# Kernel optimization log

Measured on AMD Instinct MI355X. Metric: run time of the kernel, lower is better.

Reference implementation:

```python
import jax, jax.numpy as jnp
import numpy as np

B, T, D, I, C, H = 8192, 128, 7, 128, 10, 64
L = 2 ** D
SUBSET = int(I * 0.8)  # feature_subset_size = 102


def setup_inputs() -> dict:
    key = jax.random.key(0)
    ks = jax.random.split(key, 7)
    x = jax.random.normal(ks[0], (B, I), dtype=jnp.float32)
    # exact feature-subset mask: SUBSET ones per (tree, depth) row
    r = jax.random.uniform(ks[1], (T, D, I))
    ranks = jnp.argsort(jnp.argsort(r, axis=-1), axis=-1)
    feature_mask = (ranks < SUBSET).astype(jnp.float32)
    thresholds = jax.random.normal(ks[2], (T, D), dtype=jnp.float32)
    leaf_outputs = jax.random.normal(ks[3], (T, L, C), dtype=jnp.float32)
    W1 = jax.random.normal(ks[4], (I, H), dtype=jnp.float32) * 0.08
    b1 = jnp.zeros((H,), dtype=jnp.float32)
    W2 = jax.random.normal(ks[5], (H, T), dtype=jnp.float32) * 0.12
    b2 = jnp.zeros((T,), dtype=jnp.float32)
    return {"x": x, "feature_mask": feature_mask, "thresholds": thresholds,
            "leaf_outputs": leaf_outputs, "W1": W1, "b1": b1, "W2": W2, "b2": b2}


def reference(x, feature_mask, thresholds, leaf_outputs, W1, b1, W2, b2):
    depth = thresholds.shape[1]
    # split logits: masked feature sum minus threshold, per (batch, tree, depth)
    z = jnp.einsum('bi,tdi->btd', x, feature_mask) - thresholds[None, :, :]
    s = 0.5 * (z / (1.0 + jnp.abs(z)) + 1.0)  # scaled softsign split in (0,1)
    # probabilistic path routing: doubling concat, identical to torch loop
    p = jnp.ones((x.shape[0], feature_mask.shape[0], 1), dtype=x.dtype)
    for d in range(depth):
        sd = s[:, :, d:d + 1]            # [B, T, 1]
        p = jnp.concatenate([p * sd, p * (1.0 - sd)], axis=-1)  # [B, T, 2^(d+1)]
    leaf_probs = jax.nn.softmax(leaf_outputs, axis=-1)           # [T, L, C]
    tree_outputs = jnp.einsum('btl,tlc->btc', p, leaf_probs)     # [B, T, C]
    # instance-wise attention over trees (eval mode: no dropout)
    attn = jax.nn.softmax(jax.nn.relu(x @ W1 + b1) @ W2 + b2, axis=-1)  # [B, T]
    return jnp.sum(tree_outputs * attn[:, :, None], axis=1)     # [B, C]
```

## Files before the change

### kernel.cpp

```cpp
#include <hip/hip_runtime.h>
#include <hip/hip_bf16.h>


#define BB 8192
#define TT 128
#define II 128
#define CC 10
#define HH 64

#define OFF_S   0
#define OFF_AT  7340032
#define OFF_LPB 8388608
#define OFF_PT  8650752

typedef __attribute__((ext_vector_type(8))) short short8;
typedef __attribute__((ext_vector_type(16))) float floatx16;

static __device__ inline unsigned int pkbf(float lo, float hi) {
  __hip_bfloat162 h = __float22bfloat162_rn(make_float2(lo, hi));
  unsigned int u;
  __builtin_memcpy(&u, &h, 4);
  return u;
}

static __device__ inline short8 cvt8(float4 a, float4 b) {
  union { short8 v; unsigned int u[4]; } r;
  r.u[0] = pkbf(a.x, a.y);
  r.u[1] = pkbf(a.z, a.w);
  r.u[2] = pkbf(b.x, b.y);
  r.u[3] = pkbf(b.z, b.w);
  return r.v;
}

__global__ __launch_bounds__(256, 2) void phase1_kernel(
    const float* __restrict__ x, const float* __restrict__ mask,
    const float* __restrict__ thr, const float* __restrict__ lo,
    const float* __restrict__ W1, const float* __restrict__ b1,
    const float* __restrict__ W2, const float* __restrict__ b2,
    float* __restrict__ sT, float* __restrict__ attnT,
    unsigned int* __restrict__ lpb) {
  __shared__ float smem[13728];
  const int blk = blockIdx.x;
  const int tid = threadIdx.x;

  if (blk < 512) {
    float* xsT  = smem;
    float* Ws   = smem + 2304;
    float* hids = smem + 10496;
    float* lgt  = smem + 11648;
    float* mred = smem + 13696;
    float* sred = smem + 13712;
    const int bbase = blk * 16;

#pragma unroll
    for (int j = 0; j < 2; ++j) {
      int f = tid + 256 * j;
      int r = f >> 5, k4 = f & 31;
      float4 v = *(const float4*)(x + (size_t)(bbase + r) * II + k4 * 4);
      xsT[(k4 * 4 + 0) * 18 + r] = v.x; xsT[(k4 * 4 + 1) * 18 + r] = v.y;
      xsT[(k4 * 4 + 2) * 18 + r] = v.z; xsT[(k4 * 4 + 3) * 18 + r] = v.w;
    }
#pragma unroll
    for (int j = 0; j < 8; ++j)
      ((float4*)Ws)[tid + 256 * j] = ((const float4*)W1)[tid + 256 * j];
    __syncthreads();

    const int bt = tid >> 5, ht = tid & 31;
    float bh0 = b1[ht * 2], bh1 = b1[ht * 2 + 1];
    float a00 = bh0, a01 = bh1, a10 = bh0, a11 = bh1;
#pragma unroll 8
    for (int k = 0; k < 128; ++k) {
      float2 xv = *(const float2*)&xsT[k * 18 + bt * 2];
      float2 wv = *(const float2*)&Ws[k * 64 + ht * 2];
      a00 = fmaf(xv.x, wv.x, a00); a01 = fmaf(xv.x, wv.y, a01);
      a10 = fmaf(xv.y, wv.x, a10); a11 = fmaf(xv.y, wv.y, a11);
    }
    a00 = fmaxf(a00, 0.f); a01 = fmaxf(a01, 0.f);
    a10 = fmaxf(a10, 0.f); a11 = fmaxf(a11, 0.f);
    hids[(ht * 2 + 0) * 18 + bt * 2 + 0] = a00;
    hids[(ht * 2 + 1) * 18 + bt * 2 + 0] = a01;
    hids[(ht * 2 + 0) * 18 + bt * 2 + 1] = a10;
    hids[(ht * 2 + 1) * 18 + bt * 2 + 1] = a11;
    __syncthreads();

#pragma unroll
    for (int j = 0; j < 8; ++j)
      ((float4*)Ws)[tid + 256 * j] = ((const float4*)W2)[tid + 256 * j];
    __syncthreads();

    const int bt2 = tid >> 5, tt = tid & 31;
    float l0[4], l1[4];
#pragma unroll
    for (int j = 0; j < 4; ++j) { l0[j] = b2[tt * 4 + j]; l1[j] = l0[j]; }
#pragma unroll 4
    for (int k = 0; k < 64; ++k) {
      float2 hv = *(const float2*)&hids[k * 18 + bt2 * 2];
      float4 wv = *(const float4*)&Ws[k * 128 + tt * 4];
      float w[4] = {wv.x, wv.y, wv.z, wv.w};
#pragma unroll
      for (int j = 0; j < 4; ++j) {
        l0[j] = fmaf(hv.x, w[j], l0[j]);
        l1[j] = fmaf(hv.y, w[j], l1[j]);
      }
    }
#pragma unroll
    for (int j = 0; j < 4; ++j) {
      lgt[(bt2 * 2 + 0) * 128 + tt * 4 + j] = l0[j];
      lgt[(bt2 * 2 + 1) * 128 + tt * 4 + j] = l1[j];
    }
    __syncthreads();

    if (tid < 16) {
      float m = -1e30f;
      for (int t = 0; t < TT; ++t) m = fmaxf(m, lgt[tid * 128 + t]);
      float s = 0.f;
      for (int t = 0; t < TT; ++t) s += __expf(lgt[tid * 128 + t] - m);
      mred[tid] = m; sred[tid] = 1.f / s;
    }
    __syncthreads();

#pragma unroll
    for (int j = 0; j < 8; ++j) {
      int idx = tid + 256 * j;
      int r = idx & 15, t = idx >> 4;
      float a = __expf(lgt[r * 128 + t] - mred[r]) * sred[r];
      attnT[(size_t)t * BB + bbase + r] = a;
    }

  } else if (blk < 1408) {
    const int blk2 = blk - 512;
    const int mb = blk2 >> 5;
    const int ns = blk2 & 31;
    const int w = tid >> 6, lane = tid & 63;
    const int half = lane >> 5, l31 = lane & 31;
    const int m0 = mb * 32;

    short8 af[8];
    const float* mrow = mask + (size_t)(m0 + l31) * II + half * 8;
#pragma unroll
    for (int s = 0; s < 8; ++s) {
      float4 a = *(const float4*)(mrow + s * 16);
      float4 b = *(const float4*)(mrow + s * 16 + 4);
      af[s] = cvt8(a, b);
    }
    float th[16];
#pragma unroll
    for (int r = 0; r < 16; ++r)
      th[r] = thr[m0 + (r & 3) + 8 * (r >> 2) + 4 * half];

#pragma unroll
    for (int nb = 0; nb < 2; ++nb) {
      const int n0 = ns * 256 + w * 64 + nb * 32;
      const float* xrow = x + (size_t)(n0 + l31) * II + half * 8;
      floatx16 acc;
#pragma unroll
      for (int i = 0; i < 16; ++i) acc[i] = 0.f;
#pragma unroll
      for (int s = 0; s < 8; ++s) {
        float4 a = *(const float4*)(xrow + s * 16);
        float4 b = *(const float4*)(xrow + s * 16 + 4);
        short8 bf = cvt8(a, b);
        acc = __builtin_amdgcn_mfma_f32_32x32x16_bf16(af[s], bf, acc, 0, 0, 0);
      }
#pragma unroll
      for (int r = 0; r < 16; ++r) {
        int row = (r & 3) + 8 * (r >> 2) + 4 * half;
        float z = acc[r] - th[r];
        float o = 0.5f * (z / (1.f + fabsf(z)) + 1.f);
        sT[(size_t)(m0 + row) * BB + n0 + l31] = o;
      }
    }

  } else {
    float* lps = smem;
    const int t0 = (blk - 1408) * 2;
    {
      int tl = tid >> 7, l = tid & 127;
      const float* row = lo + ((size_t)(t0 + tl) * 128 + l) * CC;
      float v[CC];
      float m = -1e30f;
#pragma unroll
      for (int c = 0; c < CC; ++c) { v[c] = row[c]; m = fmaxf(m, v[c]); }
      float s = 0.f;
#pragma unroll
      for (int c = 0; c < CC; ++c) { v[c] = __expf(v[c] - m); s += v[c]; }
      float inv = 1.f / s;
      float* o = lps + (tl * 128 + l) * 12;
#pragma unroll
      for (int c = 0; c < CC; ++c) o[c] = v[c] * inv;
      o[10] = 0.f; o[11] = 0.f;
    }
    __syncthreads();

#pragma unroll
    for (int jj = 0; jj < 4; ++jj) {
      int idx = tid + 256 * jj;
      int tl = idx >> 9, rem = idx & 511;
      int s = rem >> 6, lane = rem & 63;
      int hf = lane >> 5, n = lane & 31;
      unsigned int wd[4];
#pragma unroll
      for (int jp = 0; jp < 4; ++jp) {
        int l0 = s * 16 + hf * 8 + jp * 2;
        float f0 = (n < CC) ? lps[(tl * 128 + l0) * 12 + n] : 0.f;
        float f1 = (n < CC) ? lps[(tl * 128 + l0 + 1) * 12 + n] : 0.f;
        wd[jp] = pkbf(f0, f1);
      }
      ((uint4*)lpb)[(size_t)(t0 + tl) * 512 + s * 64 + lane] =
          make_uint4(wd[0], wd[1], wd[2], wd[3]);
    }
  }
}

__global__ __launch_bounds__(256, 4) void main_kernel(
    const float* __restrict__ sT, const float* __restrict__ attnT,
    const unsigned int* __restrict__ lpb, float* __restrict__ partial) {
  __shared__ float red[128 * 10];
  const int bg = blockIdx.x, tg = blockIdx.y;
  const int tid = threadIdx.x;
  const int w = tid >> 6, lane = tid & 63;
  const int half = lane >> 5;
  const int b = bg * 128 + w * 32 + (lane & 31);

  floatx16 acc;
#pragma unroll
  for (int i = 0; i < 16; ++i) acc[i] = 0.f;

#pragma unroll 1
  for (int it = 0; it < 8; ++it) {
    const int t = tg * 8 + it;
    uint4 bf[8];
    const uint4* lpt = (const uint4*)lpb + (size_t)t * 512 + lane;
#pragma unroll
    for (int s = 0; s < 8; ++s) bf[s] = lpt[s * 64];

    const float* sp = sT + (size_t)t * 7 * BB + b;
    float s0 = sp[0 * BB], s1 = sp[1 * BB], s2 = sp[2 * BB], s3 = sp[3 * BB];
    float s4 = sp[4 * BB], s5 = sp[5 * BB], s6 = sp[6 * BB];
    float A = attnT[(size_t)t * BB + b];

    float s0c = 1.f - s0, s1c = 1.f - s1, s2c = 1.f - s2;
    float t0 = s0 * s1, t1 = s0c * s1, t2 = s0 * s1c, t3 = s0c * s1c;
    float pl[8];
    pl[0] = t0 * s2;  pl[1] = t1 * s2;  pl[2] = t2 * s2;  pl[3] = t3 * s2;
    pl[4] = t0 * s2c; pl[5] = t1 * s2c; pl[6] = t2 * s2c; pl[7] = t3 * s2c;
    float sel3 = half ? (1.f - s3) : s3;
    float Af = A * sel3;
    float s4c = 1.f - s4, s5c = 1.f - s5;
    float as6 = Af * s6, as6c = Af * (1.f - s6);
    float u0 = s4 * s5, u1 = s4c * s5, u2 = s4 * s5c, u3 = s4c * s5c;
    float wv[8];
    wv[0] = u0 * as6;  wv[1] = u1 * as6;  wv[2] = u2 * as6;  wv[3] = u3 * as6;
    wv[4] = u0 * as6c; wv[5] = u1 * as6c; wv[6] = u2 * as6c; wv[7] = u3 * as6c;

#pragma unroll
    for (int s = 0; s < 8; ++s) {
      float ws = wv[s];
      union { short8 v; unsigned int u[4]; } a;
#pragma unroll
      for (int jp = 0; jp < 4; ++jp)
        a.u[jp] = pkbf(pl[jp * 2] * ws, pl[jp * 2 + 1] * ws);
      acc = __builtin_amdgcn_mfma_f32_32x32x16_bf16(
          a.v, *(const short8*)&bf[s], acc, 0, 0, 0);
    }
  }

  const int col = lane & 31;
  if (col < CC) {
#pragma unroll
    for (int r = 0; r < 16; ++r) {
      int row = (r & 3) + 8 * (r >> 2) + 4 * half;
      red[(w * 32 + row) * 10 + col] = acc[r];
    }
  }
  __syncthreads();
#pragma unroll
  for (int j = 0; j < 5; ++j) {
    int idx = tid + 256 * j;
    partial[(size_t)tg * 81920 + (size_t)bg * 1280 + idx] = red[idx];
  }
}

__global__ __launch_bounds__(256) void reduce_kernel(
    const float* __restrict__ partial, float* __restrict__ out) {
  int idx = blockIdx.x * 256 + threadIdx.x;
  float s = 0.f;
#pragma unroll
  for (int tg = 0; tg < 16; ++tg) s += partial[(size_t)tg * 81920 + idx];
  out[idx] = s;
}

extern "C" void kernel_launch(void* const* d_in, const int* in_sizes, int n_in,
                              void* d_out, int out_size, void* d_ws, size_t ws_size,
                              hipStream_t stream) {
  const float* x    = (const float*)d_in[0];
  const float* mask = (const float*)d_in[1];
  const float* thr  = (const float*)d_in[2];
  const float* lo   = (const float*)d_in[3];
  const float* W1   = (const float*)d_in[4];
  const float* b1   = (const float*)d_in[5];
  const float* W2   = (const float*)d_in[6];
  const float* b2   = (const float*)d_in[7];
  float* out = (float*)d_out;
  float* ws  = (float*)d_ws;

  float*        sT      = ws + OFF_S;
  float*        attnT   = ws + OFF_AT;
  unsigned int* LPb     = (unsigned int*)(ws + OFF_LPB);
  float*        partial = ws + OFF_PT;

  phase1_kernel<<<1472, 256, 0, stream>>>(x, mask, thr, lo, W1, b1, W2, b2,
                                          sT, attnT, LPb);
  main_kernel<<<dim3(64, 16), 256, 0, stream>>>(sT, attnT, LPb, partial);
  reduce_kernel<<<320, 256, 0, stream>>>(partial, out);
}
```

Baseline: 125.1 us.

## Store split probs and attention in fp16 and compute attention MLP with MFMA

The split probabilities and attention weights now go to the workspace as fp16 instead of fp32, which halves the traffic between the first kernel and the main kernel. Attention is stored batch-major, so each main_kernel thread loads its 8 values in one vector load. The attention MLP moves from scalar FMAs in shared memory to bf16 MFMA tiles, with a wave-shuffle softmax and fewer blocks. This trades precision (bf16 MLP inputs, fp16 intermediates) for less memory traffic and faster attention compute.

```diff
diff --git a/kernel.cpp b/kernel.cpp
--- a/kernel.cpp
+++ b/kernel.cpp
@@ -1,5 +1,6 @@
 #include <hip/hip_runtime.h>
 #include <hip/hip_bf16.h>
+#include <hip/hip_fp16.h>
 
 
 #define BB 8192
@@ -9,9 +10,9 @@
 #define HH 64
 
 #define OFF_S   0
-#define OFF_AT  7340032
-#define OFF_LPB 8388608
-#define OFF_PT  8650752
+#define OFF_AT  3670016
+#define OFF_LPB 4194304
+#define OFF_PT  4456448
 
 typedef __attribute__((ext_vector_type(8))) short short8;
 typedef __attribute__((ext_vector_type(16))) float floatx16;
@@ -32,117 +33,140 @@
   return r.v;
 }
 
-__global__ __launch_bounds__(256, 2) void phase1_kernel(
+__global__ __launch_bounds__(256, 4) void phase1_kernel(
     const float* __restrict__ x, const float* __restrict__ mask,
     const float* __restrict__ thr, const float* __restrict__ lo,
     const float* __restrict__ W1, const float* __restrict__ b1,
     const float* __restrict__ W2, const float* __restrict__ b2,
-    float* __restrict__ sT, float* __restrict__ attnT,
+    __half* __restrict__ sTh, __half* __restrict__ attnB,
     unsigned int* __restrict__ lpb) {
-  __shared__ float smem[13728];
+  __shared__ float smem[8704];
   const int blk = blockIdx.x;
   const int tid = threadIdx.x;
-
-  if (blk < 512) {
-    float* xsT  = smem;
-    float* Ws   = smem + 2304;
-    float* hids = smem + 10496;
-    float* lgt  = smem + 11648;
-    float* mred = smem + 13696;
-    float* sred = smem + 13712;
-    const int bbase = blk * 16;
-
-#pragma unroll
-    for (int j = 0; j < 2; ++j) {
-      int f = tid + 256 * j;
-      int r = f >> 5, k4 = f & 31;
-      float4 v = *(const float4*)(x + (size_t)(bbase + r) * II + k4 * 4);
-      xsT[(k4 * 4 + 0) * 18 + r] = v.x; xsT[(k4 * 4 + 1) * 18 + r] = v.y;
-      xsT[(k4 * 4 + 2) * 18 + r] = v.z; xsT[(k4 * 4 + 3) * 18 + r] = v.w;
-    }
-#pragma unroll
-    for (int j = 0; j < 8; ++j)
-      ((float4*)Ws)[tid + 256 * j] = ((const float4*)W1)[tid + 256 * j];
+  const int wv = tid >> 6, lane = tid & 63;
+  const int half = lane >> 5, l31 = lane & 31;
+
+  if (blk < 64) {
+    const int b0 = blk * 128 + wv * 32;
+
+    short8 axf[8];
+    const float* xrow = x + (size_t)(b0 + l31) * II + half * 8;
+#pragma unroll
+    for (int s = 0; s < 8; ++s)
+      axf[s] = cvt8(*(const float4*)(xrow + s * 16),
+                    *(const float4*)(xrow + s * 16 + 4));
+
+    floatx16 acch[2];
+#pragma unroll
+    for (int i = 0; i < 16; ++i) { acch[0][i] = 0.f; acch[1][i] = 0.f; }
+#pragma unroll
+    for (int s = 0; s < 8; ++s) {
+#pragma unroll
+      for (int tile = 0; tile < 2; ++tile) {
+        union { short8 v; unsigned int u[4]; } wf;
+#pragma unroll
+        for (int jp = 0; jp < 4; ++jp) {
+          int k0 = s * 16 + half * 8 + jp * 2;
+          float f0 = W1[(size_t)k0 * HH + tile * 32 + l31];
+          float f1 = W1[(size_t)(k0 + 1) * HH + tile * 32 + l31];
+          wf.u[jp] = pkbf(f0, f1);
+        }
+        acch[tile] = __builtin_amdgcn_mfma_f32_32x32x16_bf16(
+            axf[s], wf.v, acch[tile], 0, 0, 0);
+      }
+    }
+    float* hids = smem + wv * 2176;
+#pragma unroll
+    for (int tile = 0; tile < 2; ++tile) {
+      float bh = b1[tile * 32 + l31];
+#pragma unroll
+      for (int r = 0; r < 16; ++r) {
+        int row = (r & 3) + 8 * (r >> 2) + 4 * half;
+        hids[row * 68 + tile * 32 + l31] = fmaxf(acch[tile][r] + bh, 0.f);
+      }
+    }
     __syncthreads();
 
-    const int bt = tid >> 5, ht = tid & 31;
-    float bh0 = b1[ht * 2], bh1 = b1[ht * 2 + 1];
-    float a00 = bh0, a01 = bh1, a10 = bh0, a11 = bh1;
-#pragma unroll 8
-    for (int k = 0; k < 128; ++k) {
-      float2 xv = *(const float2*)&xsT[k * 18 + bt * 2];
-      float2 wv = *(const float2*)&Ws[k * 64 + ht * 2];
-      a00 = fmaf(xv.x, wv.x, a00); a01 = fmaf(xv.x, wv.y, a01);
-      a10 = fmaf(xv.y, wv.x, a10); a11 = fmaf(xv.y, wv.y, a11);
-    }
-    a00 = fmaxf(a00, 0.f); a01 = fmaxf(a01, 0.f);
-    a10 = fmaxf(a10, 0.f); a11 = fmaxf(a11, 0.f);
-    hids[(ht * 2 + 0) * 18 + bt * 2 + 0] = a00;
-    hids[(ht * 2 + 1) * 18 + bt * 2 + 0] = a01;
-    hids[(ht * 2 + 0) * 18 + bt * 2 + 1] = a10;
-    hids[(ht * 2 + 1) * 18 + bt * 2 + 1] = a11;
-    __syncthreads();
-
-#pragma unroll
-    for (int j = 0; j < 8; ++j)
-      ((float4*)Ws)[tid + 256 * j] = ((const float4*)W2)[tid + 256 * j];
-    __syncthreads();
-
-    const int bt2 = tid >> 5, tt = tid & 31;
-    float l0[4], l1[4];
-#pragma unroll
-    for (int j = 0; j < 4; ++j) { l0[j] = b2[tt * 4 + j]; l1[j] = l0[j]; }
-#pragma unroll 4
-    for (int k = 0; k < 64; ++k) {
-      float2 hv = *(const float2*)&hids[k * 18 + bt2 * 2];
-      float4 wv = *(const float4*)&Ws[k * 128 + tt * 4];
-      float w[4] = {wv.x, wv.y, wv.z, wv.w};
-#pragma unroll
-      for (int j = 0; j < 4; ++j) {
-        l0[j] = fmaf(hv.x, w[j], l0[j]);
-        l1[j] = fmaf(hv.y, w[j], l1[j]);
-      }
-    }
-#pragma unroll
-    for (int j = 0; j < 4; ++j) {
-      lgt[(bt2 * 2 + 0) * 128 + tt * 4 + j] = l0[j];
-      lgt[(bt2 * 2 + 1) * 128 + tt * 4 + j] = l1[j];
-    }
-    __syncthreads();
-
-    if (tid < 16) {
-      float m = -1e30f;
-      for (int t = 0; t < TT; ++t) m = fmaxf(m, lgt[tid * 128 + t]);
-      float s = 0.f;
-      for (int t = 0; t < TT; ++t) s += __expf(lgt[tid * 128 + t] - m);
-      mred[tid] = m; sred[tid] = 1.f / s;
-    }
-    __syncthreads();
-
-#pragma unroll
-    for (int j = 0; j < 8; ++j) {
-      int idx = tid + 256 * j;
-      int r = idx & 15, t = idx >> 4;
-      float a = __expf(lgt[r * 128 + t] - mred[r]) * sred[r];
-      attnT[(size_t)t * BB + bbase + r] = a;
-    }
-
-  } else if (blk < 1408) {
-    const int blk2 = blk - 512;
+    short8 ahf[4];
+#pragma unroll
+    for (int s = 0; s < 4; ++s) {
+      const float* hr = hids + l31 * 68 + s * 16 + half * 8;
+      ahf[s] = cvt8(*(const float4*)hr, *(const float4*)(hr + 4));
+    }
+
+    floatx16 accl[4];
+#pragma unroll
+    for (int tile = 0; tile < 4; ++tile) {
+#pragma unroll
+      for (int i = 0; i < 16; ++i) accl[tile][i] = 0.f;
+#pragma unroll
+      for (int s = 0; s < 4; ++s) {
+        union { short8 v; unsigned int u[4]; } wf;
+#pragma unroll
+        for (int jp = 0; jp < 4; ++jp) {
+          int k0 = s * 16 + half * 8 + jp * 2;
+          float f0 = W2[(size_t)k0 * TT + tile * 32 + l31];
+          float f1 = W2[(size_t)(k0 + 1) * TT + tile * 32 + l31];
+          wf.u[jp] = pkbf(f0, f1);
+        }
+        accl[tile] = __builtin_amdgcn_mfma_f32_32x32x16_bf16(
+            ahf[s], wf.v, accl[tile], 0, 0, 0);
+      }
+      float bt = b2[tile * 32 + l31];
+#pragma unroll
+      for (int i = 0; i < 16; ++i) accl[tile][i] += bt;
+    }
+
+    float mrow[16];
+#pragma unroll
+    for (int r = 0; r < 16; ++r)
+      mrow[r] = fmaxf(fmaxf(accl[0][r], accl[1][r]),
+                      fmaxf(accl[2][r], accl[3][r]));
+#pragma unroll
+    for (int msk = 1; msk <= 16; msk <<= 1)
+#pragma unroll
+      for (int r = 0; r < 16; ++r)
+        mrow[r] = fmaxf(mrow[r], __shfl_xor(mrow[r], msk, 64));
+    float srow[16];
+#pragma unroll
+    for (int r = 0; r < 16; ++r) srow[r] = 0.f;
+#pragma unroll
+    for (int tile = 0; tile < 4; ++tile)
+#pragma unroll
+      for (int r = 0; r < 16; ++r) {
+        float e = __expf(accl[tile][r] - mrow[r]);
+        accl[tile][r] = e;
+        srow[r] += e;
+      }
+#pragma unroll
+    for (int msk = 1; msk <= 16; msk <<= 1)
+#pragma unroll
+      for (int r = 0; r < 16; ++r)
+        srow[r] += __shfl_xor(srow[r], msk, 64);
+#pragma unroll
+    for (int r = 0; r < 16; ++r) srow[r] = 1.f / srow[r];
+
+#pragma unroll
+    for (int tile = 0; tile < 4; ++tile)
+#pragma unroll
+      for (int r = 0; r < 16; ++r) {
+        int row = (r & 3) + 8 * (r >> 2) + 4 * half;
+        attnB[(size_t)(b0 + row) * TT + tile * 32 + l31] =
+            __float2half(accl[tile][r] * srow[r]);
+      }
+
+  } else if (blk < 960) {
+    const int blk2 = blk - 64;
     const int mb = blk2 >> 5;
     const int ns = blk2 & 31;
-    const int w = tid >> 6, lane = tid & 63;
-    const int half = lane >> 5, l31 = lane & 31;
     const int m0 = mb * 32;
 
     short8 af[8];
     const float* mrow = mask + (size_t)(m0 + l31) * II + half * 8;
 #pragma unroll
-    for (int s = 0; s < 8; ++s) {
-      float4 a = *(const float4*)(mrow + s * 16);
-      float4 b = *(const float4*)(mrow + s * 16 + 4);
-      af[s] = cvt8(a, b);
-    }
+    for (int s = 0; s < 8; ++s)
+      af[s] = cvt8(*(const float4*)(mrow + s * 16),
+                   *(const float4*)(mrow + s * 16 + 4));
     float th[16];
 #pragma unroll
     for (int r = 0; r < 16; ++r)
@@ -150,16 +174,15 @@
 
 #pragma unroll
     for (int nb = 0; nb < 2; ++nb) {
-      const int n0 = ns * 256 + w * 64 + nb * 32;
+      const int n0 = ns * 256 + wv * 64 + nb * 32;
       const float* xrow = x + (size_t)(n0 + l31) * II + half * 8;
       floatx16 acc;
 #pragma unroll
       for (int i = 0; i < 16; ++i) acc[i] = 0.f;
 #pragma unroll
       for (int s = 0; s < 8; ++s) {
-        float4 a = *(const float4*)(xrow + s * 16);
-        float4 b = *(const float4*)(xrow + s * 16 + 4);
-        short8 bf = cvt8(a, b);
+        short8 bf = cvt8(*(const float4*)(xrow + s * 16),
+                         *(const float4*)(xrow + s * 16 + 4));
         acc = __builtin_amdgcn_mfma_f32_32x32x16_bf16(af[s], bf, acc, 0, 0, 0);
       }
 #pragma unroll
@@ -167,13 +190,13 @@
         int row = (r & 3) + 8 * (r >> 2) + 4 * half;
         float z = acc[r] - th[r];
         float o = 0.5f * (z / (1.f + fabsf(z)) + 1.f);
-        sT[(size_t)(m0 + row) * BB + n0 + l31] = o;
+        sTh[(size_t)(m0 + row) * BB + n0 + l31] = __float2half(o);
       }
     }
 
   } else {
     float* lps = smem;
-    const int t0 = (blk - 1408) * 2;
+    const int t0 = (blk - 960) * 2;
     {
       int tl = tid >> 7, l = tid & 127;
       const float* row = lo + ((size_t)(t0 + tl) * 128 + l) * CC;
@@ -196,8 +219,8 @@
     for (int jj = 0; jj < 4; ++jj) {
       int idx = tid + 256 * jj;
       int tl = idx >> 9, rem = idx & 511;
-      int s = rem >> 6, lane = rem & 63;
-      int hf = lane >> 5, n = lane & 31;
+      int s = rem >> 6, ln = rem & 63;
+      int hf = ln >> 5, n = ln & 31;
       unsigned int wd[4];
 #pragma unroll
       for (int jp = 0; jp < 4; ++jp) {
@@ -206,14 +229,14 @@
         float f1 = (n < CC) ? lps[(tl * 128 + l0 + 1) * 12 + n] : 0.f;
         wd[jp] = pkbf(f0, f1);
       }
-      ((uint4*)lpb)[(size_t)(t0 + tl) * 512 + s * 64 + lane] =
+      ((uint4*)lpb)[(size_t)(t0 + tl) * 512 + s * 64 + ln] =
           make_uint4(wd[0], wd[1], wd[2], wd[3]);
     }
   }
 }
 
 __global__ __launch_bounds__(256, 4) void main_kernel(
-    const float* __restrict__ sT, const float* __restrict__ attnT,
+    const __half* __restrict__ sTh, const __half* __restrict__ attnB,
     const unsigned int* __restrict__ lpb, float* __restrict__ partial) {
   __shared__ float red[128 * 10];
   const int bg = blockIdx.x, tg = blockIdx.y;
@@ -222,6 +245,9 @@
   const int half = lane >> 5;
   const int b = bg * 128 + w * 32 + (lane & 31);
 
+  __half av[8];
+  *(uint4*)av = *(const uint4*)(attnB + (size_t)b * TT + tg * 8);
+
   floatx16 acc;
 #pragma unroll
   for (int i = 0; i < 16; ++i) acc[i] = 0.f;
@@ -234,10 +260,12 @@
 #pragma unroll
     for (int s = 0; s < 8; ++s) bf[s] = lpt[s * 64];
 
-    const float* sp = sT + (size_t)t * 7 * BB + b;
-    float s0 = sp[0 * BB], s1 = sp[1 * BB], s2 = sp[2 * BB], s3 = sp[3 * BB];
-    float s4 = sp[4 * BB], s5 = sp[5 * BB], s6 = sp[6 * BB];
-    float A = attnT[(size_t)t * BB + b];
+    const __half* sp = sTh + (size_t)t * 7 * BB + b;
+    float s0 = __half2float(sp[0 * BB]), s1 = __half2float(sp[1 * BB]);
+    float s2 = __half2float(sp[2 * BB]), s3 = __half2float(sp[3 * BB]);
+    float s4 = __half2float(sp[4 * BB]), s5 = __half2float(sp[5 * BB]);
+    float s6 = __half2float(sp[6 * BB]);
+    float A = __half2float(av[it]);
 
     float s0c = 1.f - s0, s1c = 1.f - s1, s2c = 1.f - s2;
     float t0 = s0 * s1, t1 = s0c * s1, t2 = s0 * s1c, t3 = s0c * s1c;
@@ -304,13 +332,13 @@
   float* out = (float*)d_out;
   float* ws  = (float*)d_ws;
 
-  float*        sT      = ws + OFF_S;
-  float*        attnT   = ws + OFF_AT;
+  __half*       sTh     = (__half*)(ws + OFF_S);
+  __half*       attnB   = (__half*)(ws + OFF_AT);
   unsigned int* LPb     = (unsigned int*)(ws + OFF_LPB);
   float*        partial = ws + OFF_PT;
 
-  phase1_kernel<<<1472, 256, 0, stream>>>(x, mask, thr, lo, W1, b1, W2, b2,
-                                          sT, attnT, LPb);
-  main_kernel<<<dim3(64, 16), 256, 0, stream>>>(sT, attnT, LPb, partial);
+  phase1_kernel<<<1024, 256, 0, stream>>>(x, mask, thr, lo, W1, b1, W2, b2,
+                                          sTh, attnB, LPb);
+  main_kernel<<<dim3(64, 16), 256, 0, stream>>>(sTh, attnB, LPb, partial);
   reduce_kernel<<<320, 256, 0, stream>>>(partial, out);
 }
```

Measured after the change: 142.7 us. 1.14x slower.
